# Performance work log

Hardware: AMD Instinct MI355X
Metric: run time of the kernel (lower is better)

## Reference

```python
import jax, jax.numpy as jnp
import numpy as np
from jax import lax

N, XD, L, D, R = 32768, 8, 16, 64, 64
HID_E, HID_N, MIX = 256, 512, 32
LOG2PI = float(np.log(2.0 * np.pi))


def setup_inputs() -> dict:
    key = jax.random.key(0)
    ks = jax.random.split(key, 18)
    g = lambda k, shape, s: (jax.random.normal(k, shape, jnp.float32) * s)
    init_std = 0.001
    return {
        "X": jax.random.normal(ks[0], (N, XD, L), jnp.float32),
        "init_w": g(ks[1], (1, R), init_std),
        "cores": g(ks[2], (L, R, D, R), init_std),          # core_list stacked
        "enc1_w": g(ks[3], (HID_E, XD), 1.0 / np.sqrt(XD)),
        "enc1_b": jnp.zeros((HID_E,), jnp.float32),
        "enc2_w": g(ks[4], (D, HID_E), 1.0 / np.sqrt(HID_E)),
        "enc2_b": jnp.zeros((D,), jnp.float32),
        "nade_w1": g(ks[5], (HID_N, R), 1.0 / np.sqrt(R)),
        "nade_b1": jnp.zeros((HID_N,), jnp.float32),
        "nade_w2": g(ks[6], (R, HID_N), 1.0 / np.sqrt(HID_N)),
        "nade_b2": jnp.zeros((R,), jnp.float32),
        "mu_w": g(ks[7], (MIX * XD, R), 1.0 / np.sqrt(R)),
        "mu_b": jnp.zeros((MIX * XD,), jnp.float32),
        "sig_w": g(ks[8], (MIX * XD, R), 1.0 / np.sqrt(R)),
        "sig_b": jnp.zeros((MIX * XD,), jnp.float32),
        "alpha_w": g(ks[9], (MIX, R), 1.0 / np.sqrt(R)),
        "alpha_b": jnp.zeros((MIX,), jnp.float32),
    }


def _encode(x, enc1_w, enc1_b, enc2_w, enc2_b):
    # x: [..., xd] -> [..., d]  (NADE-style input encoder)
    h = jax.nn.relu(x @ enc1_w.T + enc1_b)
    return h @ enc2_w.T + enc2_b


def _phi(x, h, nade_w1, nade_b1, nade_w2, nade_b2,
         mu_w, mu_b, sig_w, sig_b, alpha_w, alpha_b):
    # x: [n, xd], h: [n, r] hidden state -> [n] mixture-of-Gaussians log-density
    n = x.shape[0]
    h = jax.nn.relu(h @ nade_w1.T + nade_b1)
    h = jax.nn.relu(h @ nade_w2.T + nade_b2)
    mu = (h @ mu_w.T + mu_b).reshape(n, MIX, XD)
    log_sig = (h @ sig_w.T + sig_b).reshape(n, MIX, XD)
    sig = jnp.exp(log_sig)
    log_alpha = jax.nn.log_softmax(h @ alpha_w.T + alpha_b, axis=-1)  # [n, MIX]
    z = (x[:, None, :] - mu) / sig
    comp_lp = jnp.sum(-0.5 * z * z - log_sig - 0.5 * LOG2PI, axis=-1)  # [n, MIX]
    return jax.nn.logsumexp(log_alpha + comp_lp, axis=-1)


def reference(X, init_w, cores, enc1_w, enc1_b, enc2_w, enc2_b,
              nade_w1, nade_b1, nade_w2, nade_b2,
              mu_w, mu_b, sig_w, sig_b, alpha_w, alpha_b):
    n = X.shape[0]
    xseq = jnp.transpose(X, (2, 0, 1))                      # [L, n, xd]
    enc_all = _encode(xseq, enc1_w, enc1_b, enc2_w, enc2_b)  # [L, n, d]
    phi = lambda x, h: _phi(x, h, nade_w1, nade_b1, nade_w2, nade_b2,
                            mu_w, mu_b, sig_w, sig_b, alpha_w, alpha_b)

    tmp0 = jnp.broadcast_to(init_w, (n, R))
    res0 = phi(xseq[0], tmp0)
    norm0 = jnp.sum(tmp0 * tmp0)

    def step(tmp, inp):
        enc_prev, core_prev, x_cur = inp
        tmp = jnp.einsum('nd,ni,idj->nj', enc_prev, tmp, core_prev)
        return tmp, (phi(x_cur, tmp), jnp.sum(tmp * tmp))

    xs = (enc_all[:L - 1], cores[:L - 1], xseq[1:])
    _, (res_steps, norm_steps) = lax.scan(step, tmp0, xs)
    result = res0 + jnp.sum(res_steps, axis=0)   # [n] log-likelihood
    norm = norm0 + jnp.sum(norm_steps)           # scalar Frobenius norm accumulator
    return result, norm
```

## Files before the change

### kernel.cpp

```cpp
#include <hip/hip_runtime.h>

typedef unsigned short u16;
typedef unsigned int u32;
typedef __attribute__((ext_vector_type(8))) __bf16 bf16x8;
typedef __attribute__((ext_vector_type(4))) float f32x4;

#define NSAMP 32768
#define HALF_LOG2PI 0.91893853320467274f

#define O_W1N 0
#define O_W2N 32768
#define O_MUW 65536
#define O_SGW 81920
#define O_ALW 98304
#define O_E1W 100352
#define O_E2W 108544
#define O_CORT 124928
#define CORT_STEP 262144

#define L_H1A 0
#define L_H1B 8192
#define L_LM1 0
#define L_LM2 1024
#define L_LS1 8192
#define L_LS2 9216
#define L_PRA 0
#define L_PRB 8192
#define L_PRC 16384
#define L_H2  16384
#define L_CLP 24576
#define L_ALP 32768
#define L_XT  40960
#define L_XP  43008
#define L_TMPA 49152
#define L_TMPB 57344
#define L_ENC 65536
#define LDS_BYTES 81920

static __device__ __forceinline__ u16 f2b(float x){ return __builtin_bit_cast(u16,(__bf16)x); }
static __device__ __forceinline__ float b2f(u16 u){ return __builtin_bit_cast(float,((u32)u)<<16); }
static __device__ __forceinline__ float b2flo(u32 v){ return __builtin_bit_cast(float, v<<16); }
static __device__ __forceinline__ float b2fhi(u32 v){ return __builtin_bit_cast(float, v & 0xffff0000u); }
static __device__ __forceinline__ u32 pk2(float lo, float hi){
  return (u32)__builtin_bit_cast(u16,(__bf16)lo) | ((u32)__builtin_bit_cast(u16,(__bf16)hi)<<16);
}
static __device__ __forceinline__ f32x4 MF(uint4 a, uint4 b, f32x4 c){
  union U{uint4 q; bf16x8 v;};
  U A, B; A.q=a; B.q=b;
  return __builtin_amdgcn_mfma_f32_16x16x32_bf16(A.v, B.v, c, 0, 0, 0);
}

__global__ void prep_w(const float* __restrict__ nw1, const float* __restrict__ nw2,
                       const float* __restrict__ muw, const float* __restrict__ sgw,
                       const float* __restrict__ alw, const float* __restrict__ e1w,
                       const float* __restrict__ e2w, u16* __restrict__ ws,
                       float* __restrict__ out) {
  int idx0 = blockIdx.x * blockDim.x + threadIdx.x;
  int stride = gridDim.x * blockDim.x;
  for (int idx = idx0; idx < 124928; idx += stride) {
    float v;
    if      (idx < 32768)  v = nw1[idx];
    else if (idx < 65536)  v = nw2[idx - 32768];
    else if (idx < 81920)  v = muw[idx - 65536];
    else if (idx < 98304)  v = sgw[idx - 81920];
    else if (idx < 100352) v = alw[idx - 98304];
    else if (idx < 108544) { int j = idx - 100352; int o = j >> 5, k = j & 31;
                             v = (k < 8) ? e1w[o*8 + k] : 0.0f; }
    else                   v = e2w[idx - 108544];
    ws[idx] = f2b(v);
  }
  if (idx0 == 0) out[NSAMP] = 0.0f;
}

__global__ void prep_core(const float* __restrict__ cores, u16* __restrict__ ws) {
  int t = blockIdx.x >> 6, i = blockIdx.x & 63;
  const float* src = cores + ((size_t)(t*64 + i) * 64) * 64;
  u16* dst = ws + O_CORT + (size_t)t * CORT_STEP;
  for (int idx = threadIdx.x; idx < 4096; idx += 256) {
    int d = idx >> 6, j = idx & 63;
    float v = src[d*64 + j];
    int k = i*64 + d;
    int kk = k >> 5, g = (k >> 3) & 3, b = k & 7;
    int ot = j >> 4, li = j & 15;
    dst[(size_t)(((kk*4 + ot)*64) + g*16 + li)*8 + b] = f2b(v);
  }
}

__global__ __launch_bounds__(256, 2)
void fused(const float* __restrict__ X, const float* __restrict__ init_w,
           const float* __restrict__ b1e, const float* __restrict__ b2e,
           const float* __restrict__ b1n, const float* __restrict__ b2n,
           const float* __restrict__ mub, const float* __restrict__ sgb,
           const float* __restrict__ alb, const u16* __restrict__ ws,
           float* __restrict__ out) {
  __shared__ __align__(16) char Lp[LDS_BYTES];
  const int tid = threadIdx.x;
  const int w = tid >> 6, l = tid & 63, li = l & 15, g = l >> 4;
  const int e3 = li & 7;
  const int sw = e3 << 4;
  const int n0 = blockIdx.x * 64;
  float res = 0.f, nrm = 0.f;

  char* TMPc = Lp + L_TMPA;
  char* TMPn = Lp + L_TMPB;

  for (int idx = tid; idx < 4096; idx += 256) {
    int s = idx >> 6, r = idx & 63;
    *(u16*)(TMPc + s*128 + ((2*r) ^ ((s & 7) << 4))) = f2b(init_w[r]);
  }
  { uint4 z = {0,0,0,0};
    *(uint4*)(Lp + L_XP + tid*16) = z; }
  if (tid < 64) { float v = init_w[tid]; nrm += 64.f * v * v; }
  __syncthreads();

  for (int t = 0; t < 16; ++t) {
    for (int idx = tid; idx < 512; idx += 256) {
      int d = idx >> 6, s = idx & 63;
      float x = X[(size_t)(n0 + s)*128 + d*16 + t];
      *(float*)(Lp + L_XT + (d*64 + s)*4) = x;
      *(u16*)(Lp + L_XP + s*64 + ((2*d) ^ ((s & 3) << 4))) = f2b(x);
    }

    f32x4 acc2[4];
#pragma unroll
    for (int st = 0; st < 4; ++st) acc2[st] = (f32x4){0.f,0.f,0.f,0.f};
#pragma unroll 1
    for (int p = 0; p <= 8; ++p) {
      if (p < 8) {
        const u16* a0p = ws + O_W1N + (p*64 + w*16 + li)*64 + 8*g;
        uint4 af0 = *(const uint4*)a0p;
        uint4 af1 = *(const uint4*)(a0p + 32);
        float4 bb = *(const float4*)(b1n + p*64 + w*16 + 4*g);
        char* H1b = Lp + ((p & 1) ? L_H1B : L_H1A);
#pragma unroll
        for (int st = 0; st < 4; ++st) {
          int s = st*16 + li;
          uint4 b0 = *(const uint4*)(TMPc + s*128 + ((16*g) ^ sw));
          uint4 b1 = *(const uint4*)(TMPc + s*128 + ((64 + 16*g) ^ sw));
          f32x4 a1 = (f32x4){0.f,0.f,0.f,0.f};
          a1 = MF(af0, b0, a1); a1 = MF(af1, b1, a1);
          float v0 = fmaxf(a1[0] + bb.x, 0.f), v1 = fmaxf(a1[1] + bb.y, 0.f);
          float v2 = fmaxf(a1[2] + bb.z, 0.f), v3 = fmaxf(a1[3] + bb.w, 0.f);
          *(u32*)(H1b + s*128 + ((32*w + 8*g) ^ sw))     = pk2(v0, v1);
          *(u32*)(H1b + s*128 + ((32*w + 8*g + 4) ^ sw)) = pk2(v2, v3);
        }
      }
      if (p > 0) {
        int q = p - 1;
        const u16* a2p = ws + O_W2N + (w*16 + li)*512 + q*64 + 8*g;
        uint4 c0 = *(const uint4*)a2p;
        uint4 c1 = *(const uint4*)(a2p + 32);
        const char* H1r = Lp + ((q & 1) ? L_H1B : L_H1A);
#pragma unroll
        for (int st = 0; st < 4; ++st) {
          int s = st*16 + li;
          uint4 b0 = *(const uint4*)(H1r + s*128 + ((16*g) ^ sw));
          uint4 b1 = *(const uint4*)(H1r + s*128 + ((64 + 16*g) ^ sw));
          acc2[st] = MF(c0, b0, acc2[st]); acc2[st] = MF(c1, b1, acc2[st]);
        }
      }
      __syncthreads();
    }
    {
      float4 bb = *(const float4*)(b2n + w*16 + 4*g);
#pragma unroll
      for (int st = 0; st < 4; ++st) {
        int s = st*16 + li;
        float v0 = fmaxf(acc2[st][0] + bb.x, 0.f), v1 = fmaxf(acc2[st][1] + bb.y, 0.f);
        float v2 = fmaxf(acc2[st][2] + bb.z, 0.f), v3 = fmaxf(acc2[st][3] + bb.w, 0.f);
        *(u32*)(Lp + L_H2 + s*128 + ((32*w + 8*g) ^ sw))     = pk2(v0, v1);
        *(u32*)(Lp + L_H2 + s*128 + ((32*w + 8*g + 4) ^ sw)) = pk2(v2, v3);
      }
    }
    __syncthreads();

#pragma unroll 1
    for (int c = 0; c < 4; ++c) {
      int ob = c*64 + w*16;
      const u16* as_ = ws + O_SGW + (ob + li)*64 + 8*g;
      const u16* am_ = ws + O_MUW + (ob + li)*64 + 8*g;
      uint4 sf0 = *(const uint4*)as_, sf1 = *(const uint4*)(as_ + 32);
      uint4 mf0 = *(const uint4*)am_, mf1 = *(const uint4*)(am_ + 32);
      float4 bs = *(const float4*)(sgb + ob + 4*g);
      float4 bm = *(const float4*)(mub + ob + 4*g);
      const float bsv[4] = {bs.x,bs.y,bs.z,bs.w};
      const float bmv[4] = {bm.x,bm.y,bm.z,bm.w};
#pragma unroll
      for (int st = 0; st < 4; ++st) {
        int s = st*16 + li;
        uint4 b0 = *(const uint4*)(Lp + L_H2 + s*128 + ((16*g) ^ sw));
        uint4 b1 = *(const uint4*)(Lp + L_H2 + s*128 + ((64 + 16*g) ^ sw));
        f32x4 aS = (f32x4){0.f,0.f,0.f,0.f}, aM = (f32x4){0.f,0.f,0.f,0.f};
        aS = MF(sf0, b0, aS); aS = MF(sf1, b1, aS);
        aM = MF(mf0, b0, aM); aM = MF(mf1, b1, aM);
        float part = 0.f;
#pragma unroll
        for (int r = 0; r < 4; ++r) {
          int d = (4*g + r) & 7;
          float ls = aS[r] + bsv[r];
          float mu = aM[r] + bmv[r];
          float xv = *(const float*)(Lp + L_XT + (d*64 + s)*4);
          float z = (xv - mu) * __expf(-ls);
          part += -0.5f*z*z - ls - HALF_LOG2PI;
        }
        float comb = part + __shfl_xor(part, 16);
        if (!(g & 1)) {
          int mix = c*8 + 2*w + (g >> 1);
          *(float*)(Lp + L_CLP + (mix*64 + s)*4) = comb;
        }
      }
    }
    {
      int s = w*16 + li;
#pragma unroll
      for (int ot = 0; ot < 2; ++ot) {
        const u16* aa = ws + O_ALW + (ot*16 + li)*64 + 8*g;
        uint4 a0 = *(const uint4*)aa, a1 = *(const uint4*)(aa + 32);
        uint4 b0 = *(const uint4*)(Lp + L_H2 + s*128 + ((16*g) ^ sw));
        uint4 b1 = *(const uint4*)(Lp + L_H2 + s*128 + ((64 + 16*g) ^ sw));
        f32x4 acc = (f32x4){0.f,0.f,0.f,0.f};
        acc = MF(a0, b0, acc); acc = MF(a1, b1, acc);
        float4 ab4 = *(const float4*)(alb + ot*16 + 4*g);
        const float abv[4] = {ab4.x, ab4.y, ab4.z, ab4.w};
#pragma unroll
        for (int r = 0; r < 4; ++r)
          *(float*)(Lp + L_ALP + ((ot*16 + 4*g + r)*64 + s)*4) = acc[r] + abv[r];
      }
    }
    __syncthreads();

    float g1, g2;
    {
      int s = l;
      float m1 = -1e30f, m2 = -1e30f;
#pragma unroll
      for (int mm = 0; mm < 8; ++mm) {
        int m = w*8 + mm;
        float a = *(const float*)(Lp + L_ALP + (m*64 + s)*4);
        float c = *(const float*)(Lp + L_CLP + (m*64 + s)*4);
        m1 = fmaxf(m1, a + c); m2 = fmaxf(m2, a);
      }
      *(float*)(Lp + L_LM1 + (w*64 + s)*4) = m1;
      *(float*)(Lp + L_LM2 + (w*64 + s)*4) = m2;
      __syncthreads();
      g1 = fmaxf(fmaxf(*(const float*)(Lp + L_LM1 + s*4),
                       *(const float*)(Lp + L_LM1 + (64 + s)*4)),
                 fmaxf(*(const float*)(Lp + L_LM1 + (128 + s)*4),
                       *(const float*)(Lp + L_LM1 + (192 + s)*4)));
      g2 = fmaxf(fmaxf(*(const float*)(Lp + L_LM2 + s*4),
                       *(const float*)(Lp + L_LM2 + (64 + s)*4)),
                 fmaxf(*(const float*)(Lp + L_LM2 + (128 + s)*4),
                       *(const float*)(Lp + L_LM2 + (192 + s)*4)));
      float s1 = 0.f, s2 = 0.f;
#pragma unroll
      for (int mm = 0; mm < 8; ++mm) {
        int m = w*8 + mm;
        float a = *(const float*)(Lp + L_ALP + (m*64 + s)*4);
        float c = *(const float*)(Lp + L_CLP + (m*64 + s)*4);
        s1 += __expf(a + c - g1); s2 += __expf(a - g2);
      }
      *(float*)(Lp + L_LS1 + (w*64 + s)*4) = s1;
      *(float*)(Lp + L_LS2 + (w*64 + s)*4) = s2;
      __syncthreads();
    }
    if (tid < 64) {
      float s1 = *(const float*)(Lp + L_LS1 + tid*4)
               + *(const float*)(Lp + L_LS1 + (64 + tid)*4)
               + *(const float*)(Lp + L_LS1 + (128 + tid)*4)
               + *(const float*)(Lp + L_LS1 + (192 + tid)*4);
      float s2 = *(const float*)(Lp + L_LS2 + tid*4)
               + *(const float*)(Lp + L_LS2 + (64 + tid)*4)
               + *(const float*)(Lp + L_LS2 + (128 + tid)*4)
               + *(const float*)(Lp + L_LS2 + (192 + tid)*4);
      res += (g1 + __logf(s1)) - (g2 + __logf(s2));
    }
    if (t == 15) break;

    f32x4 acE[4];
#pragma unroll
    for (int st = 0; st < 4; ++st) acE[st] = (f32x4){0.f,0.f,0.f,0.f};
#pragma unroll 1
    for (int p = 0; p <= 4; ++p) {
      if (p < 4) {
        const u16* aep = ws + O_E1W + (p*64 + w*16 + li)*32 + 8*g;
        uint4 ae = *(const uint4*)aep;
        float4 bb = *(const float4*)(b1e + p*64 + w*16 + 4*g);
        char* H1b = Lp + ((p & 1) ? L_H1B : L_H1A);
#pragma unroll
        for (int st = 0; st < 4; ++st) {
          int s = st*16 + li;
          uint4 b0 = *(const uint4*)(Lp + L_XP + s*64 + ((16*g) ^ ((s & 3) << 4)));
          f32x4 ah = (f32x4){0.f,0.f,0.f,0.f};
          ah = MF(ae, b0, ah);
          float v0 = fmaxf(ah[0] + bb.x, 0.f), v1 = fmaxf(ah[1] + bb.y, 0.f);
          float v2 = fmaxf(ah[2] + bb.z, 0.f), v3 = fmaxf(ah[3] + bb.w, 0.f);
          *(u32*)(H1b + s*128 + ((32*w + 8*g) ^ sw))     = pk2(v0, v1);
          *(u32*)(H1b + s*128 + ((32*w + 8*g + 4) ^ sw)) = pk2(v2, v3);
        }
      }
      if (p > 0) {
        int q = p - 1;
        const u16* c0p = ws + O_E2W + (w*16 + li)*256 + q*64 + 8*g;
        uint4 c0 = *(const uint4*)c0p, c1 = *(const uint4*)(c0p + 32);
        const char* H1r = Lp + ((q & 1) ? L_H1B : L_H1A);
#pragma unroll
        for (int st = 0; st < 4; ++st) {
          int s = st*16 + li;
          uint4 b0 = *(const uint4*)(H1r + s*128 + ((16*g) ^ sw));
          uint4 b1 = *(const uint4*)(H1r + s*128 + ((64 + 16*g) ^ sw));
          acE[st] = MF(c0, b0, acE[st]); acE[st] = MF(c1, b1, acE[st]);
        }
      }
      if (p == 4) {
        float4 be = *(const float4*)(b2e + w*16 + 4*g);
        const float bev[4] = {be.x, be.y, be.z, be.w};
#pragma unroll
        for (int st = 0; st < 4; ++st) {
          int s = st*16 + li;
#pragma unroll
          for (int r = 0; r < 4; ++r) {
            int d = w*16 + 4*g + r;
            *(float*)(Lp + L_ENC + s*256 + ((((d >> 3) ^ e3)) << 5) + ((d & 7) << 2))
                = acE[st][r] + bev[r];
          }
        }
      }
      __syncthreads();
    }

    f32x4 aU[4][4];
#pragma unroll
    for (int ot = 0; ot < 4; ++ot)
#pragma unroll
      for (int st = 0; st < 4; ++st) aU[ot][st] = (f32x4){0.f,0.f,0.f,0.f};

    const u16* Abase = ws + O_CORT + (size_t)t*CORT_STEP + (size_t)(w*32)*2048 + (size_t)l*8;
    uint4 A0 = *(const uint4*)(Abase);
    uint4 A1 = *(const uint4*)(Abase + 512);
    uint4 A2 = *(const uint4*)(Abase + 1024);
    uint4 A3 = *(const uint4*)(Abase + 1536);
#pragma unroll 1
    for (int kk = 0; kk < 32; ++kk) {
      uint4 nA0, nA1, nA2, nA3;
      if (kk < 31) {
        const u16* ap = Abase + (size_t)(kk + 1)*2048;
        nA0 = *(const uint4*)(ap);
        nA1 = *(const uint4*)(ap + 512);
        nA2 = *(const uint4*)(ap + 1024);
        nA3 = *(const uint4*)(ap + 1536);
      }
      int kwa = w*32 + kk;
      int h = kwa & 1;
      int tof = (kwa & ~1) ^ sw;
      int eof = ((((h << 2) | g) ^ e3) << 5);
      uint4 B[4];
#pragma unroll
      for (int st = 0; st < 4; ++st) {
        int s = st*16 + li;
        float ts = b2f(*(const u16*)(TMPc + s*128 + tof));
        const char* ep = Lp + L_ENC + s*256 + eof;
        float4 e0 = *(const float4*)(ep);
        float4 e1 = *(const float4*)(ep + 16);
        uint4 bb;
        bb.x = pk2(ts*e0.x, ts*e0.y); bb.y = pk2(ts*e0.z, ts*e0.w);
        bb.z = pk2(ts*e1.x, ts*e1.y); bb.w = pk2(ts*e1.z, ts*e1.w);
        B[st] = bb;
      }
      __builtin_amdgcn_s_setprio(1);
#pragma unroll
      for (int ot = 0; ot < 4; ++ot) {
        uint4 Af = (ot == 0) ? A0 : (ot == 1) ? A1 : (ot == 2) ? A2 : A3;
#pragma unroll
        for (int st = 0; st < 4; ++st)
          aU[ot][st] = MF(Af, B[st], aU[ot][st]);
      }
      __builtin_amdgcn_s_setprio(0);
      A0 = nA0; A1 = nA1; A2 = nA2; A3 = nA3;
    }

    if (w >= 2) {
      char* pr = Lp + ((w == 2) ? L_PRA : L_PRB);
#pragma unroll
      for (int ot = 0; ot < 4; ++ot)
#pragma unroll
        for (int st = 0; st < 4; ++st) {
          uint2 pv;
          pv.x = pk2(aU[ot][st][0], aU[ot][st][1]);
          pv.y = pk2(aU[ot][st][2], aU[ot][st][3]);
          *(uint2*)(pr + (st*16 + li)*128 + 8*(((ot << 2) | g) ^ e3)) = pv;
        }
    }
    __syncthreads();
    if (w < 2) {
      const char* pr = Lp + ((w == 0) ? L_PRA : L_PRB);
#pragma unroll
      for (int ot = 0; ot < 4; ++ot)
#pragma unroll
        for (int st = 0; st < 4; ++st) {
          uint2 pv = *(const uint2*)(pr + (st*16 + li)*128 + 8*(((ot << 2) | g) ^ e3));
          aU[ot][st][0] += b2flo(pv.x); aU[ot][st][1] += b2fhi(pv.x);
          aU[ot][st][2] += b2flo(pv.y); aU[ot][st][3] += b2fhi(pv.y);
        }
      int stb = (w == 0) ? 2 : 0;
#pragma unroll
      for (int sto = 0; sto < 2; ++sto) {
        int st = stb + sto;
#pragma unroll
        for (int ot = 0; ot < 4; ++ot) {
          uint2 pv;
          pv.x = pk2(aU[ot][st][0], aU[ot][st][1]);
          pv.y = pk2(aU[ot][st][2], aU[ot][st][3]);
          *(uint2*)(Lp + L_PRC + (st*16 + li)*128 + 8*(((ot << 2) | g) ^ e3)) = pv;
        }
      }
    }
    __syncthreads();
    if (w < 2) {
      int stb = (w == 0) ? 0 : 2;
#pragma unroll
      for (int sto = 0; sto < 2; ++sto) {
        int st = stb + sto;
        int s = st*16 + li;
#pragma unroll
        for (int ot = 0; ot < 4; ++ot) {
          uint2 pv = *(const uint2*)(Lp + L_PRC + (st*16 + li)*128 + 8*(((ot << 2) | g) ^ e3));
          float v0 = aU[ot][st][0] + b2flo(pv.x);
          float v1 = aU[ot][st][1] + b2fhi(pv.x);
          float v2 = aU[ot][st][2] + b2flo(pv.y);
          float v3 = aU[ot][st][3] + b2fhi(pv.y);
          nrm += v0*v0 + v1*v1 + v2*v2 + v3*v3;
          *(u32*)(TMPn + s*128 + ((32*ot + 8*g) ^ sw))     = pk2(v0, v1);
          *(u32*)(TMPn + s*128 + ((32*ot + 8*g + 4) ^ sw)) = pk2(v2, v3);
        }
      }
    }
    __syncthreads();
    { char* tt = TMPc; TMPc = TMPn; TMPn = tt; }
  }

  if (tid < 64) out[n0 + tid] = res;

  __syncthreads();
  *(float*)(Lp + tid*4) = nrm;
  __syncthreads();
  if (tid < 64) {
    float v = *(const float*)(Lp + tid*4)
            + *(const float*)(Lp + (tid + 64)*4)
            + *(const float*)(Lp + (tid + 128)*4)
            + *(const float*)(Lp + (tid + 192)*4);
#pragma unroll
    for (int off = 32; off > 0; off >>= 1) v += __shfl_down(v, off);
    if (tid == 0) atomicAdd(out + NSAMP, v);
  }
}

extern "C" void kernel_launch(void* const* d_in, const int* in_sizes, int n_in,
                              void* d_out, int out_size, void* d_ws, size_t ws_size,
                              hipStream_t stream) {
  const float* X      = (const float*)d_in[0];
  const float* init_w = (const float*)d_in[1];
  const float* cores  = (const float*)d_in[2];
  const float* e1w    = (const float*)d_in[3];
  const float* b1e    = (const float*)d_in[4];
  const float* e2w    = (const float*)d_in[5];
  const float* b2e    = (const float*)d_in[6];
  const float* nw1    = (const float*)d_in[7];
  const float* b1n    = (const float*)d_in[8];
  const float* nw2    = (const float*)d_in[9];
  const float* b2n    = (const float*)d_in[10];
  const float* muw    = (const float*)d_in[11];
  const float* mub    = (const float*)d_in[12];
  const float* sgw    = (const float*)d_in[13];
  const float* sgb    = (const float*)d_in[14];
  const float* alw    = (const float*)d_in[15];
  const float* alb    = (const float*)d_in[16];
  float* out = (float*)d_out;
  u16*   ws  = (u16*)d_ws;

  prep_w<<<64, 256, 0, stream>>>(nw1, nw2, muw, sgw, alw, e1w, e2w, ws, out);
  prep_core<<<960, 256, 0, stream>>>(cores, ws);
  fused<<<NSAMP/64, 256, 0, stream>>>(X, init_w, b1e, b2e, b1n, b2n,
                                      mub, sgb, alb, ws, out);
}
```

Baseline: 928.3 us.

## Restructure TT core contraction to per-d MFMA with output-split waves and smaller LDS

Replaces the K=4096 contraction (which built tmp⊗enc outer-product B fragments and split K across waves, then reduced the partial sums through LDS) with a loop over d. For each d a 64x64 MFMA of tmp against a transposed core slice is formed and scaled by enc[d] on the vector units, with each wave owning 16 output columns, so no cross-wave reduction is needed. The core prep is rearranged accordingly. LDS is reduced from 80KB to 52KB by reusing a single tmp buffer and dropping the fp32 x copy, and the launch bound is raised to 3 blocks per CU. The trade-off is extra VALU FMAs per MFMA output and tighter register pressure at 3 blocks per CU, which risks spills.

```diff
diff --git a/kernel.cpp b/kernel.cpp
--- a/kernel.cpp
+++ b/kernel.cpp
@@ -18,24 +18,19 @@
 #define O_CORT 124928
 #define CORT_STEP 262144
 
-#define L_H1A 0
-#define L_H1B 8192
-#define L_LM1 0
-#define L_LM2 1024
-#define L_LS1 8192
-#define L_LS2 9216
-#define L_PRA 0
-#define L_PRB 8192
-#define L_PRC 16384
-#define L_H2  16384
+#define L_TMP 0
+#define L_ENC 8192
+#define L_H1A 24576
+#define L_H1B 32768
 #define L_CLP 24576
 #define L_ALP 32768
-#define L_XT  40960
-#define L_XP  43008
-#define L_TMPA 49152
-#define L_TMPB 57344
-#define L_ENC 65536
-#define LDS_BYTES 81920
+#define L_H2  40960
+#define L_LM1 40960
+#define L_LM2 41984
+#define L_LS1 43008
+#define L_LS2 44032
+#define L_XP  49152
+#define LDS_BYTES 53248
 
 static __device__ __forceinline__ u16 f2b(float x){ return __builtin_bit_cast(u16,(__bf16)x); }
 static __device__ __forceinline__ float b2f(u16 u){ return __builtin_bit_cast(float,((u32)u)<<16); }
@@ -73,20 +68,21 @@
 }
 
 __global__ void prep_core(const float* __restrict__ cores, u16* __restrict__ ws) {
-  int t = blockIdx.x >> 6, i = blockIdx.x & 63;
-  const float* src = cores + ((size_t)(t*64 + i) * 64) * 64;
-  u16* dst = ws + O_CORT + (size_t)t * CORT_STEP;
+  int t = blockIdx.x >> 6, d = blockIdx.x & 63;
+  __shared__ float T[64][65];
   for (int idx = threadIdx.x; idx < 4096; idx += 256) {
-    int d = idx >> 6, j = idx & 63;
-    float v = src[d*64 + j];
-    int k = i*64 + d;
-    int kk = k >> 5, g = (k >> 3) & 3, b = k & 7;
-    int ot = j >> 4, li = j & 15;
-    dst[(size_t)(((kk*4 + ot)*64) + g*16 + li)*8 + b] = f2b(v);
-  }
-}
-
-__global__ __launch_bounds__(256, 2)
+    int i = idx >> 6, j = idx & 63;
+    T[i][j] = cores[((size_t)(t*64 + i)*64 + d)*64 + j];
+  }
+  __syncthreads();
+  u16* dst = ws + O_CORT + (size_t)t*CORT_STEP + (size_t)d*4096;
+  for (int idx = threadIdx.x; idx < 4096; idx += 256) {
+    int j = idx >> 6, i = idx & 63;
+    dst[j*64 + i] = f2b(T[i][j]);
+  }
+}
+
+__global__ __launch_bounds__(256, 3)
 void fused(const float* __restrict__ X, const float* __restrict__ init_w,
            const float* __restrict__ b1e, const float* __restrict__ b2e,
            const float* __restrict__ b1n, const float* __restrict__ b2n,
@@ -101,12 +97,9 @@
   const int n0 = blockIdx.x * 64;
   float res = 0.f, nrm = 0.f;
 
-  char* TMPc = Lp + L_TMPA;
-  char* TMPn = Lp + L_TMPB;
-
   for (int idx = tid; idx < 4096; idx += 256) {
     int s = idx >> 6, r = idx & 63;
-    *(u16*)(TMPc + s*128 + ((2*r) ^ ((s & 7) << 4))) = f2b(init_w[r]);
+    *(u16*)(Lp + L_TMP + s*128 + ((2*r) ^ ((s & 7) << 4))) = f2b(init_w[r]);
   }
   { uint4 z = {0,0,0,0};
     *(uint4*)(Lp + L_XP + tid*16) = z; }
@@ -117,8 +110,15 @@
     for (int idx = tid; idx < 512; idx += 256) {
       int d = idx >> 6, s = idx & 63;
       float x = X[(size_t)(n0 + s)*128 + d*16 + t];
-      *(float*)(Lp + L_XT + (d*64 + s)*4) = x;
       *(u16*)(Lp + L_XP + s*64 + ((2*d) ^ ((s & 3) << 4))) = f2b(x);
+    }
+
+    uint4 Bq0[4], Bq1[4];
+#pragma unroll
+    for (int st = 0; st < 4; ++st) {
+      int s = st*16 + li;
+      Bq0[st] = *(const uint4*)(Lp + L_TMP + s*128 + ((16*g) ^ sw));
+      Bq1[st] = *(const uint4*)(Lp + L_TMP + s*128 + ((64 + 16*g) ^ sw));
     }
 
     f32x4 acc2[4];
@@ -135,10 +135,8 @@
 #pragma unroll
         for (int st = 0; st < 4; ++st) {
           int s = st*16 + li;
-          uint4 b0 = *(const uint4*)(TMPc + s*128 + ((16*g) ^ sw));
-          uint4 b1 = *(const uint4*)(TMPc + s*128 + ((64 + 16*g) ^ sw));
           f32x4 a1 = (f32x4){0.f,0.f,0.f,0.f};
-          a1 = MF(af0, b0, a1); a1 = MF(af1, b1, a1);
+          a1 = MF(af0, Bq0[st], a1); a1 = MF(af1, Bq1[st], a1);
           float v0 = fmaxf(a1[0] + bb.x, 0.f), v1 = fmaxf(a1[1] + bb.y, 0.f);
           float v2 = fmaxf(a1[2] + bb.z, 0.f), v3 = fmaxf(a1[3] + bb.w, 0.f);
           *(u32*)(H1b + s*128 + ((32*w + 8*g) ^ sw))     = pk2(v0, v1);
@@ -173,6 +171,15 @@
       }
     }
     __syncthreads();
+
+    float xv[4][4];
+#pragma unroll
+    for (int st = 0; st < 4; ++st) {
+      int s = st*16 + li;
+      uint2 xq = *(const uint2*)(Lp + L_XP + s*64 + ((8*(g & 1)) ^ ((li & 3) << 4)));
+      xv[st][0] = b2flo(xq.x); xv[st][1] = b2fhi(xq.x);
+      xv[st][2] = b2flo(xq.y); xv[st][3] = b2fhi(xq.y);
+    }
 
 #pragma unroll 1
     for (int c = 0; c < 4; ++c) {
@@ -196,11 +203,9 @@
         float part = 0.f;
 #pragma unroll
         for (int r = 0; r < 4; ++r) {
-          int d = (4*g + r) & 7;
           float ls = aS[r] + bsv[r];
           float mu = aM[r] + bmv[r];
-          float xv = *(const float*)(Lp + L_XT + (d*64 + s)*4);
-          float z = (xv - mu) * __expf(-ls);
+          float z = (xv[st][r] - mu) * __expf(-ls);
           part += -0.5f*z*z - ls - HALF_LOG2PI;
         }
         float comb = part + __shfl_xor(part, 16);
@@ -212,12 +217,12 @@
     }
     {
       int s = w*16 + li;
+      uint4 b0 = *(const uint4*)(Lp + L_H2 + s*128 + ((16*g) ^ sw));
+      uint4 b1 = *(const uint4*)(Lp + L_H2 + s*128 + ((64 + 16*g) ^ sw));
 #pragma unroll
       for (int ot = 0; ot < 2; ++ot) {
         const u16* aa = ws + O_ALW + (ot*16 + li)*64 + 8*g;
         uint4 a0 = *(const uint4*)aa, a1 = *(const uint4*)(aa + 32);
-        uint4 b0 = *(const uint4*)(Lp + L_H2 + s*128 + ((16*g) ^ sw));
-        uint4 b1 = *(const uint4*)(Lp + L_H2 + s*128 + ((64 + 16*g) ^ sw));
         f32x4 acc = (f32x4){0.f,0.f,0.f,0.f};
         acc = MF(a0, b0, acc); acc = MF(a1, b1, acc);
         float4 ab4 = *(const float4*)(alb + ot*16 + 4*g);
@@ -275,6 +280,7 @@
       res += (g1 + __logf(s1)) - (g2 + __logf(s2));
     }
     if (t == 15) break;
+    __syncthreads();
 
     f32x4 acE[4];
 #pragma unroll
@@ -328,126 +334,64 @@
       __syncthreads();
     }
 
-    f32x4 aU[4][4];
-#pragma unroll
-    for (int ot = 0; ot < 4; ++ot)
-#pragma unroll
-      for (int st = 0; st < 4; ++st) aU[ot][st] = (f32x4){0.f,0.f,0.f,0.f};
-
-    const u16* Abase = ws + O_CORT + (size_t)t*CORT_STEP + (size_t)(w*32)*2048 + (size_t)l*8;
-    uint4 A0 = *(const uint4*)(Abase);
-    uint4 A1 = *(const uint4*)(Abase + 512);
-    uint4 A2 = *(const uint4*)(Abase + 1024);
-    uint4 A3 = *(const uint4*)(Abase + 1536);
+    f32x4 acc[4];
+#pragma unroll
+    for (int st = 0; st < 4; ++st) acc[st] = (f32x4){0.f,0.f,0.f,0.f};
+    const u16* AJ = ws + O_CORT + (size_t)t*CORT_STEP + (size_t)(w*16 + li)*64 + 8*g;
+    uint4 Ac0 = *(const uint4*)(AJ);
+    uint4 Ac1 = *(const uint4*)(AJ + 32);
 #pragma unroll 1
-    for (int kk = 0; kk < 32; ++kk) {
-      uint4 nA0, nA1, nA2, nA3;
-      if (kk < 31) {
-        const u16* ap = Abase + (size_t)(kk + 1)*2048;
-        nA0 = *(const uint4*)(ap);
-        nA1 = *(const uint4*)(ap + 512);
-        nA2 = *(const uint4*)(ap + 1024);
-        nA3 = *(const uint4*)(ap + 1536);
-      }
-      int kwa = w*32 + kk;
-      int h = kwa & 1;
-      int tof = (kwa & ~1) ^ sw;
-      int eof = ((((h << 2) | g) ^ e3) << 5);
-      uint4 B[4];
-#pragma unroll
-      for (int st = 0; st < 4; ++st) {
-        int s = st*16 + li;
-        float ts = b2f(*(const u16*)(TMPc + s*128 + tof));
-        const char* ep = Lp + L_ENC + s*256 + eof;
-        float4 e0 = *(const float4*)(ep);
-        float4 e1 = *(const float4*)(ep + 16);
-        uint4 bb;
-        bb.x = pk2(ts*e0.x, ts*e0.y); bb.y = pk2(ts*e0.z, ts*e0.w);
-        bb.z = pk2(ts*e1.x, ts*e1.y); bb.w = pk2(ts*e1.z, ts*e1.w);
-        B[st] = bb;
-      }
-      __builtin_amdgcn_s_setprio(1);
-#pragma unroll
-      for (int ot = 0; ot < 4; ++ot) {
-        uint4 Af = (ot == 0) ? A0 : (ot == 1) ? A1 : (ot == 2) ? A2 : A3;
-#pragma unroll
-        for (int st = 0; st < 4; ++st)
-          aU[ot][st] = MF(Af, B[st], aU[ot][st]);
-      }
-      __builtin_amdgcn_s_setprio(0);
-      A0 = nA0; A1 = nA1; A2 = nA2; A3 = nA3;
-    }
-
-    if (w >= 2) {
-      char* pr = Lp + ((w == 2) ? L_PRA : L_PRB);
-#pragma unroll
-      for (int ot = 0; ot < 4; ++ot)
-#pragma unroll
-        for (int st = 0; st < 4; ++st) {
-          uint2 pv;
-          pv.x = pk2(aU[ot][st][0], aU[ot][st][1]);
-          pv.y = pk2(aU[ot][st][2], aU[ot][st][3]);
-          *(uint2*)(pr + (st*16 + li)*128 + 8*(((ot << 2) | g) ^ e3)) = pv;
-        }
+    for (int dg = 0; dg < 16; ++dg) {
+      f32x4 E[4];
+#pragma unroll
+      for (int st = 0; st < 4; ++st)
+        E[st] = *(const f32x4*)(Lp + L_ENC + (st*16 + li)*256 +
+                                (((dg >> 1) ^ e3) << 5) + ((dg & 1) << 4));
+#pragma unroll
+      for (int dd = 0; dd < 4; ++dd) {
+        uint4 An0 = Ac0, An1 = Ac1;
+        if (dd < 3 || dg < 15) {
+          const u16* ap = AJ + (size_t)(dg*4 + dd + 1)*4096;
+          An0 = *(const uint4*)(ap);
+          An1 = *(const uint4*)(ap + 32);
+        }
+        __builtin_amdgcn_s_setprio(1);
+#pragma unroll
+        for (int st = 0; st < 4; ++st) {
+          f32x4 y = (f32x4){0.f,0.f,0.f,0.f};
+          y = MF(Ac0, Bq0[st], y);
+          y = MF(Ac1, Bq1[st], y);
+          float e = E[st][dd];
+          acc[st][0] += e * y[0]; acc[st][1] += e * y[1];
+          acc[st][2] += e * y[2]; acc[st][3] += e * y[3];
+        }
+        __builtin_amdgcn_s_setprio(0);
+        Ac0 = An0; Ac1 = An1;
+      }
+    }
+#pragma unroll
+    for (int st = 0; st < 4; ++st) {
+      int s = st*16 + li;
+      nrm += acc[st][0]*acc[st][0] + acc[st][1]*acc[st][1]
+           + acc[st][2]*acc[st][2] + acc[st][3]*acc[st][3];
+      uint2 pv;
+      pv.x = pk2(acc[st][0], acc[st][1]);
+      pv.y = pk2(acc[st][2], acc[st][3]);
+      *(uint2*)(Lp + L_TMP + s*128 + ((32*w + 8*g) ^ sw)) = pv;
     }
     __syncthreads();
-    if (w < 2) {
-      const char* pr = Lp + ((w == 0) ? L_PRA : L_PRB);
-#pragma unroll
-      for (int ot = 0; ot < 4; ++ot)
-#pragma unroll
-        for (int st = 0; st < 4; ++st) {
-          uint2 pv = *(const uint2*)(pr + (st*16 + li)*128 + 8*(((ot << 2) | g) ^ e3));
-          aU[ot][st][0] += b2flo(pv.x); aU[ot][st][1] += b2fhi(pv.x);
-          aU[ot][st][2] += b2flo(pv.y); aU[ot][st][3] += b2fhi(pv.y);
-        }
-      int stb = (w == 0) ? 2 : 0;
-#pragma unroll
-      for (int sto = 0; sto < 2; ++sto) {
-        int st = stb + sto;
-#pragma unroll
-        for (int ot = 0; ot < 4; ++ot) {
-          uint2 pv;
-          pv.x = pk2(aU[ot][st][0], aU[ot][st][1]);
-          pv.y = pk2(aU[ot][st][2], aU[ot][st][3]);
-          *(uint2*)(Lp + L_PRC + (st*16 + li)*128 + 8*(((ot << 2) | g) ^ e3)) = pv;
-        }
-      }
-    }
-    __syncthreads();
-    if (w < 2) {
-      int stb = (w == 0) ? 0 : 2;
-#pragma unroll
-      for (int sto = 0; sto < 2; ++sto) {
-        int st = stb + sto;
-        int s = st*16 + li;
-#pragma unroll
-        for (int ot = 0; ot < 4; ++ot) {
-          uint2 pv = *(const uint2*)(Lp + L_PRC + (st*16 + li)*128 + 8*(((ot << 2) | g) ^ e3));
-          float v0 = aU[ot][st][0] + b2flo(pv.x);
-          float v1 = aU[ot][st][1] + b2fhi(pv.x);
-          float v2 = aU[ot][st][2] + b2flo(pv.y);
-          float v3 = aU[ot][st][3] + b2fhi(pv.y);
-          nrm += v0*v0 + v1*v1 + v2*v2 + v3*v3;
-          *(u32*)(TMPn + s*128 + ((32*ot + 8*g) ^ sw))     = pk2(v0, v1);
-          *(u32*)(TMPn + s*128 + ((32*ot + 8*g + 4) ^ sw)) = pk2(v2, v3);
-        }
-      }
-    }
-    __syncthreads();
-    { char* tt = TMPc; TMPc = TMPn; TMPn = tt; }
   }
 
   if (tid < 64) out[n0 + tid] = res;
 
   __syncthreads();
-  *(float*)(Lp + tid*4) = nrm;
+  *(float*)(Lp + L_H1A + tid*4) = nrm;
   __syncthreads();
   if (tid < 64) {
-    float v = *(const float*)(Lp + tid*4)
-            + *(const float*)(Lp + (tid + 64)*4)
-            + *(const float*)(Lp + (tid + 128)*4)
-            + *(const float*)(Lp + (tid + 192)*4);
+    float v = *(const float*)(Lp + L_H1A + tid*4)
+            + *(const float*)(Lp + L_H1A + (tid + 64)*4)
+            + *(const float*)(Lp + L_H1A + (tid + 128)*4)
+            + *(const float*)(Lp + L_H1A + (tid + 192)*4);
 #pragma unroll
     for (int off = 32; off > 0; off >>= 1) v += __shfl_down(v, off);
     if (tid == 0) atomicAdd(out + NSAMP, v);
```

Measured after the change: 906.0 us. -2.4%, faster.
